# Optimization experiments

Measured on AMD Instinct MI355X. Metric: run time of the kernel, lower is better.

The kernel has to match this reference:

```python
import math
import jax, jax.numpy as jnp
import numpy as np

DIM = 128
NUM_PROJ = 256
ENC = jnp.asarray(2 ** np.arange(8), dtype=jnp.uint8)  # [1,2,4,...,128]
DEQUANT_SCALE = math.sqrt(math.pi / 2) / NUM_PROJ


def quantize_packed(x, S):
    # x: (..., dim) float32 -> packed uint8 (..., ceil(num_proj/8))
    projected = jnp.einsum('...d,pd->...p', x, S)
    signs = projected > 0  # bool (..., num_proj)
    pad_len = (-NUM_PROJ) % 8
    if pad_len > 0:
        pad = [(0, 0)] * (signs.ndim - 1) + [(0, pad_len)]
        signs = jnp.pad(signs, pad, constant_values=False)
    signs = signs.reshape(*signs.shape[:-1], -1, 8)  # (..., nbytes, 8)
    packed = jnp.sum(signs.astype(jnp.uint8) * ENC, axis=-1, dtype=jnp.uint8)
    return packed


def unpack_signs(packed):
    # packed: uint8 (..., nbytes) -> {-1,+1} float32 (..., num_proj)
    bits = jnp.bitwise_and(packed[..., None], ENC) > 0  # (..., nbytes, 8)
    bits = bits.reshape(*packed.shape[:-1], -1)[..., :NUM_PROJ]
    return bits.astype(jnp.float32) * 2.0 - 1.0


def setup_inputs() -> dict:
    key = jax.random.key(0)
    k1, k2, k3 = jax.random.split(key, 3)
    query = jax.random.normal(k1, (2, 32, 4096, DIM), dtype=jnp.float32)
    key_t = jax.random.normal(k2, (2, 32, 4096, DIM), dtype=jnp.float32)
    S = jax.random.normal(k3, (NUM_PROJ, DIM), dtype=jnp.float32)
    return {"query": query, "key": key_t, "S": S}


def reference(query, key, S):
    # quantize keys to bit-packed sign sketch, then estimate <query, key>
    packed = quantize_packed(key, S)                       # uint8 (..., 32)
    signs = unpack_signs(packed)                           # (..., 256)
    q_proj = jnp.einsum('...d,pd->...p', query, S)         # (..., 256)
    est = DEQUANT_SCALE * jnp.sum(q_proj * signs, axis=-1) # (B,H,S)
    return est
```

## Files before the change

kernel.cpp:

```cpp
#include <hip/hip_runtime.h>
#include <stdint.h>

#define DIM 128
#define NPROJ 256
#define TPB 128
#define TAU 0.016f
#define QCAP 512
#define DEQ 0.004895758348888673f

typedef _Float16 f16x8 __attribute__((ext_vector_type(8)));
typedef float f32x4 __attribute__((ext_vector_type(4)));

__global__ __launch_bounds__(256) void qjl_prep(const float* __restrict__ Sg,
                                                _Float16* __restrict__ ws) {
    int t = blockIdx.x * 256 + threadIdx.x;
    int lane = t & 63, fid = t >> 6;
    int f = fid & 1, ks = (fid >> 1) & 3, c = fid >> 3;
    int p = c * 32 + f * 16 + (lane & 15);
    int d0 = ks * 32 + (lane >> 4) * 8;
    const float4* s4 = (const float4*)(Sg + p * DIM + d0);
    float4 a = s4[0], b = s4[1];
    f16x8 h = {(_Float16)a.x, (_Float16)a.y, (_Float16)a.z, (_Float16)a.w,
               (_Float16)b.x, (_Float16)b.y, (_Float16)b.z, (_Float16)b.w};
    *(f16x8*)(ws + (size_t)fid * 512 + lane * 8) = h;
}

#define LOADT(buf, C, T)                                                             \
    { _Pragma("unroll")                                                              \
      for (int ks = 0; ks < 4; ++ks)                                                 \
          buf[ks] = *(const f16x8*)(ws + (size_t)((C) * 8 + ks * 2 + (T)) * 512 + lane * 8); }

#define LOADA(src)                                                                   \
    { _Pragma("unroll")                                                              \
      for (int rb = 0; rb < 2; ++rb) {                                               \
          const float* rp = (src) + (tok0 + wv * 32 + rb * 16 + m) * DIM;            \
          _Pragma("unroll")                                                          \
          for (int ks = 0; ks < 4; ++ks) {                                           \
              int d0 = ks * 32 + quad * 8;                                           \
              float4 x = *(const float4*)(rp + d0);                                  \
              float4 y = *(const float4*)(rp + d0 + 4);                              \
              af[rb][ks] = (f16x8){(_Float16)x.x, (_Float16)x.y, (_Float16)x.z, (_Float16)x.w, \
                                   (_Float16)y.x, (_Float16)y.y, (_Float16)y.z, (_Float16)y.w}; } } }

#define K_STEP(C, T, buf)                                                            \
    { f32x4 a0 = {0,0,0,0}, a1 = {0,0,0,0};                                          \
      _Pragma("unroll")                                                              \
      for (int ks = 0; ks < 4; ++ks) {                                               \
          a0 = __builtin_amdgcn_mfma_f32_16x16x32_f16(af[0][ks], buf[ks], a0, 0,0,0);\
          a1 = __builtin_amdgcn_mfma_f32_16x16x32_f16(af[1][ks], buf[ks], a1, 0,0,0);\
      }                                                                              \
      _Pragma("unroll")                                                              \
      for (int r = 0; r < 4; ++r) {                                                  \
          const int bidx = (C) * 8 + (T) * 4 + r;                                    \
          float kv0 = a0[r], kv1 = a1[r];                                            \
          sb0[bidx >> 5] |= (kv0 > 0.f) ? (1u << (bidx & 31)) : 0u;                  \
          sb1[bidx >> 5] |= (kv1 > 0.f) ? (1u << (bidx & 31)) : 0u;                  \
          if (__builtin_expect(fabsf(kv0) < TAU, 0)) {                               \
              int idx = atomicAdd(&qn, 1);                                           \
              if (idx < QCAP) qmeta[idx] = (uint32_t)(wv * 32 + quad * 4 + r)        \
                  | ((uint32_t)((C) * 32 + (T) * 16 + m) << 8)                       \
                  | ((kv0 > 0.f ? 1u : 0u) << 16);                                   \
          }                                                                          \
          if (__builtin_expect(fabsf(kv1) < TAU, 0)) {                               \
              int idx = atomicAdd(&qn, 1);                                           \
              if (idx < QCAP) qmeta[idx] = (uint32_t)(wv * 32 + 16 + quad * 4 + r)   \
                  | ((uint32_t)((C) * 32 + (T) * 16 + m) << 8)                       \
                  | ((kv1 > 0.f ? 1u : 0u) << 16);                                   \
          } } }

#define Q_STEP(C, T, buf)                                                            \
    { f32x4 a0 = {0,0,0,0}, a1 = {0,0,0,0};                                          \
      _Pragma("unroll")                                                              \
      for (int ks = 0; ks < 4; ++ks) {                                               \
          a0 = __builtin_amdgcn_mfma_f32_16x16x32_f16(af[0][ks], buf[ks], a0, 0,0,0);\
          a1 = __builtin_amdgcn_mfma_f32_16x16x32_f16(af[1][ks], buf[ks], a1, 0,0,0);\
      }                                                                              \
      _Pragma("unroll")                                                              \
      for (int r = 0; r < 4; ++r) {                                                  \
          const int bidx = (C) * 8 + (T) * 4 + r;                                    \
          est[r]     += ((sb0[bidx >> 5] >> (bidx & 31)) & 1u) ? a0[r] : -a0[r];     \
          est[4 + r] += ((sb1[bidx >> 5] >> (bidx & 31)) & 1u) ? a1[r] : -a1[r]; } }

__global__ __launch_bounds__(256, 2) void qjl_main(
    const float* __restrict__ qg, const float* __restrict__ kg,
    const float* __restrict__ Sg, const _Float16* __restrict__ ws,
    float* __restrict__ out)
{
    __shared__ float    est_s[TPB];
    __shared__ uint32_t qmeta[QCAP];
    __shared__ int      qn;

    const int tid = threadIdx.x, lane = tid & 63, wv = tid >> 6;
    const int m = lane & 15, quad = lane >> 4;
    const long tok0 = (long)blockIdx.x * TPB;
    if (tid == 0) qn = 0;
    __syncthreads();

    f16x8 af[2][4];
    f16x8 tA[4], tB[4];
    uint32_t sb0[2] = {0u, 0u}, sb1[2] = {0u, 0u};

    LOADT(tA, 0, 0);
    LOADA(kg);
    LOADT(tB, 0, 1);
    K_STEP(0, 0, tA); LOADT(tA, 1, 0);
    K_STEP(0, 1, tB); LOADT(tB, 1, 1);
    K_STEP(1, 0, tA); LOADT(tA, 2, 0);
    K_STEP(1, 1, tB); LOADT(tB, 2, 1);
    K_STEP(2, 0, tA); LOADT(tA, 3, 0);
    K_STEP(2, 1, tB); LOADT(tB, 3, 1);
    K_STEP(3, 0, tA); LOADT(tA, 4, 0);
    K_STEP(3, 1, tB); LOADT(tB, 4, 1);
    K_STEP(4, 0, tA); LOADT(tA, 5, 0);
    K_STEP(4, 1, tB); LOADT(tB, 5, 1);
    K_STEP(5, 0, tA); LOADT(tA, 6, 0);
    K_STEP(5, 1, tB); LOADT(tB, 6, 1);
    K_STEP(6, 0, tA); LOADT(tA, 7, 0);
    K_STEP(6, 1, tB); LOADT(tB, 7, 1);
    K_STEP(7, 0, tA);
    K_STEP(7, 1, tB);

    float est[8] = {0.f, 0.f, 0.f, 0.f, 0.f, 0.f, 0.f, 0.f};
    LOADT(tA, 0, 0);
    LOADA(qg);
    LOADT(tB, 0, 1);
    Q_STEP(0, 0, tA); LOADT(tA, 1, 0);
    Q_STEP(0, 1, tB); LOADT(tB, 1, 1);
    Q_STEP(1, 0, tA); LOADT(tA, 2, 0);
    Q_STEP(1, 1, tB); LOADT(tB, 2, 1);
    Q_STEP(2, 0, tA); LOADT(tA, 3, 0);
    Q_STEP(2, 1, tB); LOADT(tB, 3, 1);
    Q_STEP(3, 0, tA); LOADT(tA, 4, 0);
    Q_STEP(3, 1, tB); LOADT(tB, 4, 1);
    Q_STEP(4, 0, tA); LOADT(tA, 5, 0);
    Q_STEP(4, 1, tB); LOADT(tB, 5, 1);
    Q_STEP(5, 0, tA); LOADT(tA, 6, 0);
    Q_STEP(5, 1, tB); LOADT(tB, 6, 1);
    Q_STEP(6, 0, tA); LOADT(tA, 7, 0);
    Q_STEP(6, 1, tB); LOADT(tB, 7, 1);
    Q_STEP(7, 0, tA);
    Q_STEP(7, 1, tB);

    #pragma unroll
    for (int rb = 0; rb < 2; ++rb) {
        #pragma unroll
        for (int r = 0; r < 4; ++r) {
            float e = est[rb * 4 + r];
            e += __shfl_xor(e, 1);
            e += __shfl_xor(e, 2);
            e += __shfl_xor(e, 4);
            e += __shfl_xor(e, 8);
            if (m == 0) est_s[wv * 32 + rb * 16 + quad * 4 + r] = DEQ * e;
        }
    }
    __syncthreads();

    int nc = qn < QCAP ? qn : QCAP;
    for (int i = tid; i < nc; i += 256) {
        uint32_t mm = qmeta[i];
        int tl = mm & 255;
        int p  = (mm >> 8) & 255;
        int sf = (mm >> 16) & 1;
        const float4* kr = (const float4*)(kg + (tok0 + tl) * DIM);
        const float4* qr = (const float4*)(qg + (tok0 + tl) * DIM);
        const float4* sr = (const float4*)(Sg + (long)p * DIM);
        double dk = 0.0, dq = 0.0;
        #pragma unroll 8
        for (int j = 0; j < 32; ++j) {
            float4 kv4 = kr[j], qv4 = qr[j], sv4 = sr[j];
            dk += (double)kv4.x * (double)sv4.x + (double)kv4.y * (double)sv4.y
                + (double)kv4.z * (double)sv4.z + (double)kv4.w * (double)sv4.w;
            dq += (double)qv4.x * (double)sv4.x + (double)qv4.y * (double)sv4.y
                + (double)qv4.z * (double)sv4.z + (double)qv4.w * (double)sv4.w;
        }
        int st = (dk > 0.0) ? 1 : 0;
        if (st != sf) {
            float sg = sf ? 1.f : -1.f;
            atomicAdd(&est_s[tl], -2.f * DEQ * (float)dq * sg);
        }
    }
    __syncthreads();

    if (tid < TPB) out[tok0 + tid] = est_s[tid];
}

extern "C" void kernel_launch(void* const* d_in, const int* in_sizes, int n_in,
                              void* d_out, int out_size, void* d_ws, size_t ws_size,
                              hipStream_t stream) {
    const float* q = (const float*)d_in[0];
    const float* k = (const float*)d_in[1];
    const float* S = (const float*)d_in[2];
    float* out = (float*)d_out;
    _Float16* ws = (_Float16*)d_ws;
    hipLaunchKernelGGL(qjl_prep, dim3(16), dim3(256), 0, stream, S, ws);
    int nblocks = out_size / TPB;
    hipLaunchKernelGGL(qjl_main, dim3(nblocks), dim3(256), 0, stream, q, k, S, ws, out);
}
```

Baseline: 324.1 us.

## Fuse key and query projection passes into one sweep over S tiles

Loads both key and query fragments up front and computes their projections in the same MFMA loop, so the projection matrix tiles are streamed once instead of twice. Sign application becomes a bitwise XOR of the key sign bit into the query projection, which removes the packed sign bitmask. Launch bounds move from 2 to 3 blocks per CU to raise occupancy. In exchange each thread holds twice the A-fragment registers, which under the tighter register budget risks spilling, and all global loads are issued before any compute.

Result: slower. 419.0 us (+29.3%).

```diff
diff --git a/kernel.cpp b/kernel.cpp
--- a/kernel.cpp
+++ b/kernel.cpp
@@ -30,7 +30,7 @@
       for (int ks = 0; ks < 4; ++ks)                                                 \
           buf[ks] = *(const f16x8*)(ws + (size_t)((C) * 8 + ks * 2 + (T)) * 512 + lane * 8); }
 
-#define LOADA(src)                                                                   \
+#define LOADA(dst, src)                                                              \
     { _Pragma("unroll")                                                              \
       for (int rb = 0; rb < 2; ++rb) {                                               \
           const float* rp = (src) + (tok0 + wv * 32 + rb * 16 + m) * DIM;            \
@@ -39,49 +39,38 @@
               int d0 = ks * 32 + quad * 8;                                           \
               float4 x = *(const float4*)(rp + d0);                                  \
               float4 y = *(const float4*)(rp + d0 + 4);                              \
-              af[rb][ks] = (f16x8){(_Float16)x.x, (_Float16)x.y, (_Float16)x.z, (_Float16)x.w, \
-                                   (_Float16)y.x, (_Float16)y.y, (_Float16)y.z, (_Float16)y.w}; } } }
+              dst[rb][ks] = (f16x8){(_Float16)x.x, (_Float16)x.y, (_Float16)x.z, (_Float16)x.w, \
+                                    (_Float16)y.x, (_Float16)y.y, (_Float16)y.z, (_Float16)y.w}; } } }
 
-#define K_STEP(C, T, buf)                                                            \
-    { f32x4 a0 = {0,0,0,0}, a1 = {0,0,0,0};                                          \
+#define F_STEP(C, T, buf)                                                            \
+    { f32x4 k0 = {0,0,0,0}, k1 = {0,0,0,0}, q0 = {0,0,0,0}, q1 = {0,0,0,0};          \
       _Pragma("unroll")                                                              \
       for (int ks = 0; ks < 4; ++ks) {                                               \
-          a0 = __builtin_amdgcn_mfma_f32_16x16x32_f16(af[0][ks], buf[ks], a0, 0,0,0);\
-          a1 = __builtin_amdgcn_mfma_f32_16x16x32_f16(af[1][ks], buf[ks], a1, 0,0,0);\
+          k0 = __builtin_amdgcn_mfma_f32_16x16x32_f16(ak[0][ks], buf[ks], k0, 0,0,0);\
+          k1 = __builtin_amdgcn_mfma_f32_16x16x32_f16(ak[1][ks], buf[ks], k1, 0,0,0);\
+          q0 = __builtin_amdgcn_mfma_f32_16x16x32_f16(aq[0][ks], buf[ks], q0, 0,0,0);\
+          q1 = __builtin_amdgcn_mfma_f32_16x16x32_f16(aq[1][ks], buf[ks], q1, 0,0,0);\
       }                                                                              \
       _Pragma("unroll")                                                              \
       for (int r = 0; r < 4; ++r) {                                                  \
-          const int bidx = (C) * 8 + (T) * 4 + r;                                    \
-          float kv0 = a0[r], kv1 = a1[r];                                            \
-          sb0[bidx >> 5] |= (kv0 > 0.f) ? (1u << (bidx & 31)) : 0u;                  \
-          sb1[bidx >> 5] |= (kv1 > 0.f) ? (1u << (bidx & 31)) : 0u;                  \
-          if (__builtin_expect(fabsf(kv0) < TAU, 0)) {                               \
+          uint32_t s0 = __float_as_uint(k0[r]) & 0x80000000u;                        \
+          uint32_t s1 = __float_as_uint(k1[r]) & 0x80000000u;                        \
+          est[r]     += __uint_as_float(__float_as_uint(q0[r]) ^ s0);                \
+          est[4 + r] += __uint_as_float(__float_as_uint(q1[r]) ^ s1);                \
+          if (__builtin_expect(fabsf(k0[r]) < TAU, 0)) {                             \
               int idx = atomicAdd(&qn, 1);                                           \
               if (idx < QCAP) qmeta[idx] = (uint32_t)(wv * 32 + quad * 4 + r)        \
                   | ((uint32_t)((C) * 32 + (T) * 16 + m) << 8)                       \
-                  | ((kv0 > 0.f ? 1u : 0u) << 16);                                   \
+                  | ((s0 ? 0u : 1u) << 16);                                          \
           }                                                                          \
-          if (__builtin_expect(fabsf(kv1) < TAU, 0)) {                               \
+          if (__builtin_expect(fabsf(k1[r]) < TAU, 0)) {                             \
               int idx = atomicAdd(&qn, 1);                                           \
               if (idx < QCAP) qmeta[idx] = (uint32_t)(wv * 32 + 16 + quad * 4 + r)   \
                   | ((uint32_t)((C) * 32 + (T) * 16 + m) << 8)                       \
-                  | ((kv1 > 0.f ? 1u : 0u) << 16);                                   \
+                  | ((s1 ? 0u : 1u) << 16);                                          \
           } } }
 
-#define Q_STEP(C, T, buf)                                                            \
-    { f32x4 a0 = {0,0,0,0}, a1 = {0,0,0,0};                                          \
-      _Pragma("unroll")                                                              \
-      for (int ks = 0; ks < 4; ++ks) {                                               \
-          a0 = __builtin_amdgcn_mfma_f32_16x16x32_f16(af[0][ks], buf[ks], a0, 0,0,0);\
-          a1 = __builtin_amdgcn_mfma_f32_16x16x32_f16(af[1][ks], buf[ks], a1, 0,0,0);\
-      }                                                                              \
-      _Pragma("unroll")                                                              \
-      for (int r = 0; r < 4; ++r) {                                                  \
-          const int bidx = (C) * 8 + (T) * 4 + r;                                    \
-          est[r]     += ((sb0[bidx >> 5] >> (bidx & 31)) & 1u) ? a0[r] : -a0[r];     \
-          est[4 + r] += ((sb1[bidx >> 5] >> (bidx & 31)) & 1u) ? a1[r] : -a1[r]; } }
-
-__global__ __launch_bounds__(256, 2) void qjl_main(
+__global__ __launch_bounds__(256, 3) void qjl_main(
     const float* __restrict__ qg, const float* __restrict__ kg,
     const float* __restrict__ Sg, const _Float16* __restrict__ ws,
     float* __restrict__ out)
@@ -96,50 +85,30 @@
     if (tid == 0) qn = 0;
     __syncthreads();
 
-    f16x8 af[2][4];
+    f16x8 ak[2][4], aq[2][4];
     f16x8 tA[4], tB[4];
-    uint32_t sb0[2] = {0u, 0u}, sb1[2] = {0u, 0u};
+    float est[8] = {0.f, 0.f, 0.f, 0.f, 0.f, 0.f, 0.f, 0.f};
 
     LOADT(tA, 0, 0);
-    LOADA(kg);
+    LOADA(ak, kg);
+    LOADA(aq, qg);
     LOADT(tB, 0, 1);
-    K_STEP(0, 0, tA); LOADT(tA, 1, 0);
-    K_STEP(0, 1, tB); LOADT(tB, 1, 1);
-    K_STEP(1, 0, tA); LOADT(tA, 2, 0);
-    K_STEP(1, 1, tB); LOADT(tB, 2, 1);
-    K_STEP(2, 0, tA); LOADT(tA, 3, 0);
-    K_STEP(2, 1, tB); LOADT(tB, 3, 1);
-    K_STEP(3, 0, tA); LOADT(tA, 4, 0);
-    K_STEP(3, 1, tB); LOADT(tB, 4, 1);
-    K_STEP(4, 0, tA); LOADT(tA, 5, 0);
-    K_STEP(4, 1, tB); LOADT(tB, 5, 1);
-    K_STEP(5, 0, tA); LOADT(tA, 6, 0);
-    K_STEP(5, 1, tB); LOADT(tB, 6, 1);
-    K_STEP(6, 0, tA); LOADT(tA, 7, 0);
-    K_STEP(6, 1, tB); LOADT(tB, 7, 1);
-    K_STEP(7, 0, tA);
-    K_STEP(7, 1, tB);
-
-    float est[8] = {0.f, 0.f, 0.f, 0.f, 0.f, 0.f, 0.f, 0.f};
-    LOADT(tA, 0, 0);
-    LOADA(qg);
-    LOADT(tB, 0, 1);
-    Q_STEP(0, 0, tA); LOADT(tA, 1, 0);
-    Q_STEP(0, 1, tB); LOADT(tB, 1, 1);
-    Q_STEP(1, 0, tA); LOADT(tA, 2, 0);
-    Q_STEP(1, 1, tB); LOADT(tB, 2, 1);
-    Q_STEP(2, 0, tA); LOADT(tA, 3, 0);
-    Q_STEP(2, 1, tB); LOADT(tB, 3, 1);
-    Q_STEP(3, 0, tA); LOADT(tA, 4, 0);
-    Q_STEP(3, 1, tB); LOADT(tB, 4, 1);
-    Q_STEP(4, 0, tA); LOADT(tA, 5, 0);
-    Q_STEP(4, 1, tB); LOADT(tB, 5, 1);
-    Q_STEP(5, 0, tA); LOADT(tA, 6, 0);
-    Q_STEP(5, 1, tB); LOADT(tB, 6, 1);
-    Q_STEP(6, 0, tA); LOADT(tA, 7, 0);
-    Q_STEP(6, 1, tB); LOADT(tB, 7, 1);
-    Q_STEP(7, 0, tA);
-    Q_STEP(7, 1, tB);
+    F_STEP(0, 0, tA); LOADT(tA, 1, 0);
+    F_STEP(0, 1, tB); LOADT(tB, 1, 1);
+    F_STEP(1, 0, tA); LOADT(tA, 2, 0);
+    F_STEP(1, 1, tB); LOADT(tB, 2, 1);
+    F_STEP(2, 0, tA); LOADT(tA, 3, 0);
+    F_STEP(2, 1, tB); LOADT(tB, 3, 1);
+    F_STEP(3, 0, tA); LOADT(tA, 4, 0);
+    F_STEP(3, 1, tB); LOADT(tB, 4, 1);
+    F_STEP(4, 0, tA); LOADT(tA, 5, 0);
+    F_STEP(4, 1, tB); LOADT(tB, 5, 1);
+    F_STEP(5, 0, tA); LOADT(tA, 6, 0);
+    F_STEP(5, 1, tB); LOADT(tB, 6, 1);
+    F_STEP(6, 0, tA); LOADT(tA, 7, 0);
+    F_STEP(6, 1, tB); LOADT(tB, 7, 1);
+    F_STEP(7, 0, tA);
+    F_STEP(7, 1, tB);
 
     #pragma unroll
     for (int rb = 0; rb < 2; ++rb) {
```
